# Optimization experiments

Measured on AMD Instinct MI355X. Metric: run time of the kernel, lower is better.

The kernel has to match this reference:

```python
import jax, jax.numpy as jnp
import numpy as np

# Module / grid constants (match init_kwargs and chosen input scale)
B, H, W = 2, 512, 512
SIZE, NIN, NOUT = 3, 64, 64
STRIDE, INV_STRIDE = 1, 1
N_NZ = 131072   # active input cells
N_MASK = 131072 # active output (mask) cells


def setup_inputs() -> dict:
    key = jax.random.key(0)
    ks = jax.random.split(key, 10)
    values = jax.random.normal(ks[0], (N_NZ, NIN), dtype=jnp.float32)
    # init matches torch: uniform in [-stdv, stdv]
    stdv = 1.0 / np.sqrt(float(SIZE * SIZE * NIN))
    kernel = (jax.random.uniform(ks[1], (SIZE, SIZE, NIN, NOUT), dtype=jnp.float32) - 0.5) * 2.0 * stdv
    bias = (jax.random.uniform(ks[2], (NOUT,), dtype=jnp.float32) - 0.5) * 2.0 * stdv
    ib = jax.random.randint(ks[3], (N_NZ,), 0, B)
    iy = jax.random.randint(ks[4], (N_NZ,), 0, H)
    ix = jax.random.randint(ks[5], (N_NZ,), 0, W)
    indices = jnp.stack([ib, iy, ix], axis=1).astype(jnp.int64)  # [N,3] like input.indices().T
    mb = jax.random.randint(ks[6], (N_MASK,), 0, B)
    my = jax.random.randint(ks[7], (N_MASK,), 0, H * INV_STRIDE // STRIDE)
    mx = jax.random.randint(ks[8], (N_MASK,), 0, W * INV_STRIDE // STRIDE)
    mask_indices = jnp.stack([mb, my, mx], axis=1).astype(jnp.int64)
    mask_values = jnp.ones((N_MASK, 1), dtype=jnp.float32)
    return {"values": values, "kernel": kernel, "bias": bias,
            "mask_values": mask_values, "indices": indices, "mask_indices": mask_indices}


def reference(values, kernel, bias, mask_values, indices, mask_indices):
    # Sparse octree conv: per kernel tap, gather-matmul-scatter with index
    # shift/scale and clamping to the output grid (clamped taps pile up on
    # the border exactly as torch.maximum/minimum do in the original).
    Ho = H // STRIDE * INV_STRIDE
    Wo = W // STRIDE * INV_STRIDE
    half = SIZE // 2
    b = indices[:, 0]
    dense = jnp.zeros((B, Ho, Wo, NOUT), dtype=values.dtype)
    for ky in range(SIZE):
        for kx in range(SIZE):
            v = values @ kernel[ky, kx]  # [N, nout]
            sy = jnp.clip((indices[:, 1] * INV_STRIDE + (ky - half)) // STRIDE, 0, Ho - 1)
            sx = jnp.clip((indices[:, 2] * INV_STRIDE + (kx - half)) // STRIDE, 0, Wo - 1)
            dense = dense.at[b, sy, sx].add(v)  # scatter-add == coalesce-sum
    # densified mask (duplicates sum, matching COO coalesce semantics)
    mask = jnp.zeros((B, Ho, Wo, 1), dtype=values.dtype)
    mask = mask.at[mask_indices[:, 0], mask_indices[:, 1], mask_indices[:, 2]].add(mask_values)
    # result = (result + mask * bias) * mask  (with_bias=True, mask nonempty)
    out = (dense + mask * bias) * mask
    return out
```

## Files before the change

### kernel.cpp

```cpp
#include <hip/hip_runtime.h>

#define BATCH 2
#define HH 512
#define WW 512
#define NIN 64
#define NOUT 64
#define N_NZ 131072
#define N_MASK 131072
#define NPIX (BATCH * HH * WW)
#define PPW 64
#define MAX_ALIVE N_MASK

#define WS_MASK_OFF   256
#define WS_SLOT_OFF   (WS_MASK_OFF + (size_t)NPIX * 4)
#define WS_CMP_OFF    (WS_SLOT_OFF + (size_t)NPIX * 4)
#define WS_NEED       (WS_CMP_OFF + (size_t)MAX_ALIVE * NOUT * 4)

__global__ void mask_scatter_kernel(const float* __restrict__ mv,
                                    const int* __restrict__ midx,
                                    float* __restrict__ mask) {
    int n = blockIdx.x * blockDim.x + threadIdx.x;
    if (n < N_MASK) {
        int b = midx[n * 3 + 0];
        int y = midx[n * 3 + 1];
        int x = midx[n * 3 + 2];
        atomicAdd(&mask[(b * HH + y) * WW + x], mv[n]);
    }
}

__global__ __launch_bounds__(256) void build_slot2_kernel(
        const float* __restrict__ mask,
        int* __restrict__ slot,
        int* __restrict__ counter) {
    const int tid = threadIdx.x;
    const int gid = blockIdx.x * 256 + tid;
    const float4 m = reinterpret_cast<const float4*>(mask)[gid];
    const int c0 = (m.x != 0.f) + (m.y != 0.f) + (m.z != 0.f) + (m.w != 0.f);

    const int lane = tid & 63;
    const int wv = tid >> 6;
    int pre = c0;
#pragma unroll
    for (int d = 1; d < 64; d <<= 1) {
        int t = __shfl_up(pre, d);
        if (lane >= d) pre += t;
    }

    __shared__ int wsum[4];
    __shared__ int wbase[4];
    __shared__ int blockbase;
    if (lane == 63) wsum[wv] = pre;
    __syncthreads();
    if (tid == 0) {
        int s = 0;
#pragma unroll
        for (int w = 0; w < 4; ++w) { wbase[w] = s; s += wsum[w]; }
        blockbase = atomicAdd(counter, s);
    }
    __syncthreads();

    int s0 = blockbase + wbase[wv] + (pre - c0);
    int4 sv;
    sv.x = (m.x != 0.f) ? s0++ : -1;
    sv.y = (m.y != 0.f) ? s0++ : -1;
    sv.z = (m.z != 0.f) ? s0++ : -1;
    sv.w = (m.w != 0.f) ? s0++ : -1;
    reinterpret_cast<int4*>(slot)[gid] = sv;
}

__global__ __launch_bounds__(64, 2) void conv_scatter2_kernel(
        const float* __restrict__ values,
        const float* __restrict__ kern,
        const int* __restrict__ idx,
        const int* __restrict__ slot,
        float* __restrict__ compact) {
    const int bid  = blockIdx.x;
    const int tap  = bid % 9;
    const int tile = bid / 9;
    const int lane = threadIdx.x;
    const int ky = tap / 3;
    const int kx = tap % 3;

    float kreg[NIN];
    const float* kp = kern + (size_t)tap * NIN * NOUT + lane;
#pragma unroll
    for (int i = 0; i < NIN; ++i) kreg[i] = kp[(size_t)i * NOUT];

    const int p0 = tile * PPW;
    const int p  = p0 + lane;
    const int b = idx[p * 3 + 0];
    const int y = idx[p * 3 + 1];
    const int x = idx[p * 3 + 2];
    const int sy = min(max(y + ky - 1, 0), HH - 1);
    const int sx = min(max(x + kx - 1, 0), WW - 1);
    const int pix = (b * HH + sy) * WW + sx;
    const int s = slot[pix];

    unsigned long long alive = __ballot(s >= 0);
    while (alive) {
        const int j = __ffsll((long long)alive) - 1;
        alive &= alive - 1;
        const int sj = __shfl(s, j);
        const float* vp = values + (size_t)(p0 + j) * NIN;
        float acc = 0.0f;
#pragma unroll
        for (int i = 0; i < NIN; ++i) acc = fmaf(vp[i], kreg[i], acc);
        atomicAdd(&compact[(size_t)sj * NOUT + lane], acc);
    }
}

__global__ void finalize2_kernel(float* __restrict__ out,
                                 const float* __restrict__ mask,
                                 const int* __restrict__ slot,
                                 const float* __restrict__ compact,
                                 const float* __restrict__ bias) {
    const int t = blockIdx.x * blockDim.x + threadIdx.x;
    const int p = t >> 4;
    const int c4 = (t & 15) * 4;
    if (p >= NPIX) return;
    float4* o = reinterpret_cast<float4*>(out + (size_t)p * NOUT + c4);
    const int s = slot[p];
    if (s < 0) {
        *o = make_float4(0.f, 0.f, 0.f, 0.f);
        return;
    }
    const float m = mask[p];
    const float4 bb = *reinterpret_cast<const float4*>(bias + c4);
    float4 v = *reinterpret_cast<const float4*>(compact + (size_t)s * NOUT + c4);
    v.x = (v.x + m * bb.x) * m;
    v.y = (v.y + m * bb.y) * m;
    v.z = (v.z + m * bb.z) * m;
    v.w = (v.w + m * bb.w) * m;
    *o = v;
}

__global__ __launch_bounds__(64, 2) void conv_scatter_kernel(
        const float* __restrict__ values,
        const float* __restrict__ kern,
        const int* __restrict__ idx,
        const float* __restrict__ mask,
        float* __restrict__ dense) {
    const int bid  = blockIdx.x;
    const int tap  = bid % 9;
    const int tile = bid / 9;
    const int lane = threadIdx.x;
    const int ky = tap / 3;
    const int kx = tap % 3;
    float kreg[NIN];
    const float* kp = kern + (size_t)tap * NIN * NOUT + lane;
#pragma unroll
    for (int i = 0; i < NIN; ++i) kreg[i] = kp[(size_t)i * NOUT];
    const int p0 = tile * PPW;
    for (int pp = 0; pp < PPW; ++pp) {
        const int p = p0 + pp;
        const int b = idx[p * 3 + 0];
        const int y = idx[p * 3 + 1];
        const int x = idx[p * 3 + 2];
        const int sy = min(max(y + ky - 1, 0), HH - 1);
        const int sx = min(max(x + kx - 1, 0), WW - 1);
        const size_t pix = ((size_t)b * HH + sy) * WW + sx;
        if (mask[pix] != 0.0f) {
            const float* vp = values + (size_t)p * NIN;
            float acc = 0.0f;
#pragma unroll
            for (int i = 0; i < NIN; ++i) acc = fmaf(vp[i], kreg[i], acc);
            atomicAdd(&dense[pix * NOUT + lane], acc);
        }
    }
}

__global__ void finalize_kernel(float* __restrict__ out,
                                const float* __restrict__ mask,
                                const float* __restrict__ bias) {
    const int t = blockIdx.x * blockDim.x + threadIdx.x;
    const int p = t >> 4;
    const int c4 = (t & 15) * 4;
    if (p >= NPIX) return;
    const float m = mask[p];
    if (m == 0.0f) return;
    float4* o = reinterpret_cast<float4*>(out + (size_t)p * NOUT + c4);
    const float4 bb = *reinterpret_cast<const float4*>(bias + c4);
    float4 v = *o;
    v.x = (v.x + m * bb.x) * m;
    v.y = (v.y + m * bb.y) * m;
    v.z = (v.z + m * bb.z) * m;
    v.w = (v.w + m * bb.w) * m;
    *o = v;
}

extern "C" void kernel_launch(void* const* d_in, const int* in_sizes, int n_in,
                              void* d_out, int out_size, void* d_ws, size_t ws_size,
                              hipStream_t stream) {
    const float* values      = (const float*)d_in[0];
    const float* kern        = (const float*)d_in[1];
    const float* bias        = (const float*)d_in[2];
    const float* mask_values = (const float*)d_in[3];
    const int*   indices     = (const int*)d_in[4];
    const int*   mask_idx    = (const int*)d_in[5];
    float* out = (float*)d_out;

    if (ws_size >= WS_NEED) {
        char* ws = (char*)d_ws;
        int*   counter = (int*)ws;
        float* mask    = (float*)(ws + WS_MASK_OFF);
        int*   slot    = (int*)(ws + WS_SLOT_OFF);
        float* compact = (float*)(ws + WS_CMP_OFF);

        hipMemsetAsync(ws, 0, WS_NEED, stream);

        mask_scatter_kernel<<<(N_MASK + 255) / 256, 256, 0, stream>>>(
            mask_values, mask_idx, mask);
        build_slot2_kernel<<<NPIX / 4 / 256, 256, 0, stream>>>(
            mask, slot, counter);

        const int nblocks = 9 * (N_NZ / PPW);
        conv_scatter2_kernel<<<nblocks, 64, 0, stream>>>(
            values, kern, indices, slot, compact);

        const int total = NPIX * (NOUT / 4);
        finalize2_kernel<<<(total + 255) / 256, 256, 0, stream>>>(
            out, mask, slot, compact, bias);
    } else {
        float* mask = (float*)d_ws;
        hipMemsetAsync(out, 0, (size_t)out_size * sizeof(float), stream);
        hipMemsetAsync(mask, 0, (size_t)NPIX * sizeof(float), stream);
        mask_scatter_kernel<<<(N_MASK + 255) / 256, 256, 0, stream>>>(
            mask_values, mask_idx, mask);
        const int nblocks = 9 * (N_NZ / PPW);
        conv_scatter_kernel<<<nblocks, 64, 0, stream>>>(
            values, kern, indices, mask, out);
        const int total = NPIX * (NOUT / 4);
        finalize_kernel<<<(total + 255) / 256, 256, 0, stream>>>(out, mask, bias);
    }
}
```

Measured before the change: 267.2 us.

## Compute per-tap gather GEMMs with bf16 MFMA, converting weights once per launch

Replaces the per-tap scalar FMA kernel with a single kernel in which each wave loads 16 input rows once, converts them to bf16, and loops over all 9 taps. For each tap it runs 16x16x32 bf16 MFMAs against a pre-transposed bf16 kernel, then atomically scatters the results to compact output slots. Taps where no row in the wave hits an active output are skipped. This removes the redundant per-tap reloads of values and the scalar FMA work, but lowers input precision to bf16 and adds a small weight-conversion kernel.

```diff
diff --git a/kernel.cpp b/kernel.cpp
--- a/kernel.cpp
+++ b/kernel.cpp
@@ -8,13 +8,23 @@
 #define N_NZ 131072
 #define N_MASK 131072
 #define NPIX (BATCH * HH * WW)
-#define PPW 64
 #define MAX_ALIVE N_MASK
 
 #define WS_MASK_OFF   256
 #define WS_SLOT_OFF   (WS_MASK_OFF + (size_t)NPIX * 4)
 #define WS_CMP_OFF    (WS_SLOT_OFF + (size_t)NPIX * 4)
-#define WS_NEED       (WS_CMP_OFF + (size_t)MAX_ALIVE * NOUT * 4)
+#define WS_KT_OFF     (WS_CMP_OFF + (size_t)MAX_ALIVE * NOUT * 4)
+#define WS_NEED2      (WS_KT_OFF + (size_t)9 * NIN * NOUT * 2)
+#define WS_NEED_R5    WS_KT_OFF
+
+typedef short s8v  __attribute__((ext_vector_type(8)));
+typedef float f4v  __attribute__((ext_vector_type(4)));
+
+__device__ __forceinline__ short f2bf(float f) {
+    unsigned u = __builtin_bit_cast(unsigned, f);
+    unsigned r = u + 0x7FFFu + ((u >> 16) & 1u);
+    return (short)(r >> 16);
+}
 
 __global__ void mask_scatter_kernel(const float* __restrict__ mv,
                                     const int* __restrict__ midx,
@@ -68,44 +78,89 @@
     reinterpret_cast<int4*>(slot)[gid] = sv;
 }
 
-__global__ __launch_bounds__(64, 2) void conv_scatter2_kernel(
+__global__ void convert_kt_kernel(const float* __restrict__ kern,
+                                  short* __restrict__ kt) {
+    int t = blockIdx.x * 256 + threadIdx.x;
+    if (t < 9 * NIN * NOUT) {
+        int tap = t >> 12;
+        int rem = t & 4095;
+        int c = rem >> 6;
+        int i = rem & 63;
+        kt[tap * 4096 + c * 64 + i] = f2bf(kern[tap * 4096 + i * 64 + c]);
+    }
+}
+
+__global__ __launch_bounds__(256) void conv_mfma_kernel(
         const float* __restrict__ values,
-        const float* __restrict__ kern,
+        const short* __restrict__ kt,
         const int* __restrict__ idx,
         const int* __restrict__ slot,
         float* __restrict__ compact) {
-    const int bid  = blockIdx.x;
-    const int tap  = bid % 9;
-    const int tile = bid / 9;
-    const int lane = threadIdx.x;
-    const int ky = tap / 3;
-    const int kx = tap % 3;
-
-    float kreg[NIN];
-    const float* kp = kern + (size_t)tap * NIN * NOUT + lane;
-#pragma unroll
-    for (int i = 0; i < NIN; ++i) kreg[i] = kp[(size_t)i * NOUT];
-
-    const int p0 = tile * PPW;
-    const int p  = p0 + lane;
-    const int b = idx[p * 3 + 0];
-    const int y = idx[p * 3 + 1];
-    const int x = idx[p * 3 + 2];
-    const int sy = min(max(y + ky - 1, 0), HH - 1);
-    const int sx = min(max(x + kx - 1, 0), WW - 1);
-    const int pix = (b * HH + sy) * WW + sx;
-    const int s = slot[pix];
-
-    unsigned long long alive = __ballot(s >= 0);
-    while (alive) {
-        const int j = __ffsll((long long)alive) - 1;
-        alive &= alive - 1;
-        const int sj = __shfl(s, j);
-        const float* vp = values + (size_t)(p0 + j) * NIN;
-        float acc = 0.0f;
-#pragma unroll
-        for (int i = 0; i < NIN; ++i) acc = fmaf(vp[i], kreg[i], acc);
-        atomicAdd(&compact[(size_t)sj * NOUT + lane], acc);
+    const int wid  = threadIdx.x >> 6;
+    const int lane = threadIdx.x & 63;
+    const int q    = lane >> 4;
+    const int col  = lane & 15;
+    const int p0   = blockIdx.x * 64 + wid * 16;
+
+    const float* vrow = values + (size_t)(p0 + col) * NIN + q * 8;
+    s8v a0, a1;
+#pragma unroll
+    for (int j = 0; j < 8; ++j) {
+        a0[j] = f2bf(vrow[j]);
+        a1[j] = f2bf(vrow[32 + j]);
+    }
+
+    const int pme = p0 + col;
+    const int b = idx[pme * 3 + 0];
+    const int y = idx[pme * 3 + 1];
+    const int x = idx[pme * 3 + 2];
+
+    for (int tap = 0; tap < 9; ++tap) {
+        const int ky = tap / 3;
+        const int kx = tap % 3;
+        const int sy = min(max(y + ky - 1, 0), HH - 1);
+        const int sx = min(max(x + kx - 1, 0), WW - 1);
+        const int s = slot[(b * HH + sy) * WW + sx];
+
+        if (__ballot(s >= 0) == 0ULL) continue;
+
+        const short* ktt = kt + tap * 4096;
+        const short* kb = ktt + col * 64 + q * 8;
+
+        f4v c0 = {0.f, 0.f, 0.f, 0.f};
+        f4v c1 = {0.f, 0.f, 0.f, 0.f};
+        f4v c2 = {0.f, 0.f, 0.f, 0.f};
+        f4v c3 = {0.f, 0.f, 0.f, 0.f};
+
+        s8v b0a = *(const s8v*)(kb + 0 * 16 * 64);
+        s8v b0b = *(const s8v*)(kb + 0 * 16 * 64 + 32);
+        c0 = __builtin_amdgcn_mfma_f32_16x16x32_bf16(a0, b0a, c0, 0, 0, 0);
+        c0 = __builtin_amdgcn_mfma_f32_16x16x32_bf16(a1, b0b, c0, 0, 0, 0);
+        s8v b1a = *(const s8v*)(kb + 1 * 16 * 64);
+        s8v b1b = *(const s8v*)(kb + 1 * 16 * 64 + 32);
+        c1 = __builtin_amdgcn_mfma_f32_16x16x32_bf16(a0, b1a, c1, 0, 0, 0);
+        c1 = __builtin_amdgcn_mfma_f32_16x16x32_bf16(a1, b1b, c1, 0, 0, 0);
+        s8v b2a = *(const s8v*)(kb + 2 * 16 * 64);
+        s8v b2b = *(const s8v*)(kb + 2 * 16 * 64 + 32);
+        c2 = __builtin_amdgcn_mfma_f32_16x16x32_bf16(a0, b2a, c2, 0, 0, 0);
+        c2 = __builtin_amdgcn_mfma_f32_16x16x32_bf16(a1, b2b, c2, 0, 0, 0);
+        s8v b3a = *(const s8v*)(kb + 3 * 16 * 64);
+        s8v b3b = *(const s8v*)(kb + 3 * 16 * 64 + 32);
+        c3 = __builtin_amdgcn_mfma_f32_16x16x32_bf16(a0, b3a, c3, 0, 0, 0);
+        c3 = __builtin_amdgcn_mfma_f32_16x16x32_bf16(a1, b3b, c3, 0, 0, 0);
+
+#pragma unroll
+        for (int r = 0; r < 4; ++r) {
+            const int mr = q * 4 + r;
+            const int sr = __shfl(s, mr);
+            if (sr >= 0) {
+                float* dst = compact + (size_t)sr * NOUT + col;
+                atomicAdd(dst + 0,  c0[r]);
+                atomicAdd(dst + 16, c1[r]);
+                atomicAdd(dst + 32, c2[r]);
+                atomicAdd(dst + 48, c3[r]);
+            }
+        }
     }
 }
 
@@ -134,12 +189,12 @@
     *o = v;
 }
 
-__global__ __launch_bounds__(64, 2) void conv_scatter_kernel(
+__global__ __launch_bounds__(64, 2) void conv_scatter3_kernel(
         const float* __restrict__ values,
         const float* __restrict__ kern,
         const int* __restrict__ idx,
-        const float* __restrict__ mask,
-        float* __restrict__ dense) {
+        const int* __restrict__ slot,
+        float* __restrict__ compact) {
     const int bid  = blockIdx.x;
     const int tap  = bid % 9;
     const int tile = bid / 9;
@@ -150,42 +205,26 @@
     const float* kp = kern + (size_t)tap * NIN * NOUT + lane;
 #pragma unroll
     for (int i = 0; i < NIN; ++i) kreg[i] = kp[(size_t)i * NOUT];
-    const int p0 = tile * PPW;
-    for (int pp = 0; pp < PPW; ++pp) {
-        const int p = p0 + pp;
-        const int b = idx[p * 3 + 0];
-        const int y = idx[p * 3 + 1];
-        const int x = idx[p * 3 + 2];
-        const int sy = min(max(y + ky - 1, 0), HH - 1);
-        const int sx = min(max(x + kx - 1, 0), WW - 1);
-        const size_t pix = ((size_t)b * HH + sy) * WW + sx;
-        if (mask[pix] != 0.0f) {
-            const float* vp = values + (size_t)p * NIN;
-            float acc = 0.0f;
-#pragma unroll
-            for (int i = 0; i < NIN; ++i) acc = fmaf(vp[i], kreg[i], acc);
-            atomicAdd(&dense[pix * NOUT + lane], acc);
-        }
-    }
-}
-
-__global__ void finalize_kernel(float* __restrict__ out,
-                                const float* __restrict__ mask,
-                                const float* __restrict__ bias) {
-    const int t = blockIdx.x * blockDim.x + threadIdx.x;
-    const int p = t >> 4;
-    const int c4 = (t & 15) * 4;
-    if (p >= NPIX) return;
-    const float m = mask[p];
-    if (m == 0.0f) return;
-    float4* o = reinterpret_cast<float4*>(out + (size_t)p * NOUT + c4);
-    const float4 bb = *reinterpret_cast<const float4*>(bias + c4);
-    float4 v = *o;
-    v.x = (v.x + m * bb.x) * m;
-    v.y = (v.y + m * bb.y) * m;
-    v.z = (v.z + m * bb.z) * m;
-    v.w = (v.w + m * bb.w) * m;
-    *o = v;
+    const int p0 = tile * 64;
+    const int p  = p0 + lane;
+    const int b = idx[p * 3 + 0];
+    const int y = idx[p * 3 + 1];
+    const int x = idx[p * 3 + 2];
+    const int sy = min(max(y + ky - 1, 0), HH - 1);
+    const int sx = min(max(x + kx - 1, 0), WW - 1);
+    const int pix = (b * HH + sy) * WW + sx;
+    const int s = slot[pix];
+    unsigned long long alive = __ballot(s >= 0);
+    while (alive) {
+        const int j = __ffsll((long long)alive) - 1;
+        alive &= alive - 1;
+        const int sj = __shfl(s, j);
+        const float* vp = values + (size_t)(p0 + j) * NIN;
+        float acc = 0.0f;
+#pragma unroll
+        for (int i = 0; i < NIN; ++i) acc = fmaf(vp[i], kreg[i], acc);
+        atomicAdd(&compact[(size_t)sj * NOUT + lane], acc);
+    }
 }
 
 extern "C" void kernel_launch(void* const* d_in, const int* in_sizes, int n_in,
@@ -199,37 +238,34 @@
     const int*   mask_idx    = (const int*)d_in[5];
     float* out = (float*)d_out;
 
-    if (ws_size >= WS_NEED) {
-        char* ws = (char*)d_ws;
-        int*   counter = (int*)ws;
-        float* mask    = (float*)(ws + WS_MASK_OFF);
-        int*   slot    = (int*)(ws + WS_SLOT_OFF);
-        float* compact = (float*)(ws + WS_CMP_OFF);
-
-        hipMemsetAsync(ws, 0, WS_NEED, stream);
-
-        mask_scatter_kernel<<<(N_MASK + 255) / 256, 256, 0, stream>>>(
-            mask_values, mask_idx, mask);
-        build_slot2_kernel<<<NPIX / 4 / 256, 256, 0, stream>>>(
-            mask, slot, counter);
-
-        const int nblocks = 9 * (N_NZ / PPW);
-        conv_scatter2_kernel<<<nblocks, 64, 0, stream>>>(
+    char* ws = (char*)d_ws;
+    int*   counter = (int*)ws;
+    float* mask    = (float*)(ws + WS_MASK_OFF);
+    int*   slot    = (int*)(ws + WS_SLOT_OFF);
+    float* compact = (float*)(ws + WS_CMP_OFF);
+    short* kt      = (short*)(ws + WS_KT_OFF);
+
+    const bool mfma_path = (ws_size >= WS_NEED2);
+    const size_t zero_span = mfma_path ? WS_NEED2 : WS_NEED_R5;
+
+    hipMemsetAsync(ws, 0, zero_span, stream);
+
+    mask_scatter_kernel<<<(N_MASK + 255) / 256, 256, 0, stream>>>(
+        mask_values, mask_idx, mask);
+    build_slot2_kernel<<<NPIX / 4 / 256, 256, 0, stream>>>(
+        mask, slot, counter);
+
+    if (mfma_path) {
+        convert_kt_kernel<<<(9 * NIN * NOUT + 255) / 256, 256, 0, stream>>>(
+            kern, kt);
+        conv_mfma_kernel<<<N_NZ / 64, 256, 0, stream>>>(
+            values, kt, indices, slot, compact);
+    } else {
+        conv_scatter3_kernel<<<9 * (N_NZ / 64), 64, 0, stream>>>(
             values, kern, indices, slot, compact);
-
-        const int total = NPIX * (NOUT / 4);
-        finalize2_kernel<<<(total + 255) / 256, 256, 0, stream>>>(
-            out, mask, slot, compact, bias);
-    } else {
-        float* mask = (float*)d_ws;
-        hipMemsetAsync(out, 0, (size_t)out_size * sizeof(float), stream);
-        hipMemsetAsync(mask, 0, (size_t)NPIX * sizeof(float), stream);
-        mask_scatter_kernel<<<(N_MASK + 255) / 256, 256, 0, stream>>>(
-            mask_values, mask_idx, mask);
-        const int nblocks = 9 * (N_NZ / PPW);
-        conv_scatter_kernel<<<nblocks, 64, 0, stream>>>(
-            values, kern, indices, mask, out);
-        const int total = NPIX * (NOUT / 4);
-        finalize_kernel<<<(total + 255) / 256, 256, 0, stream>>>(out, mask, bias);
-    }
-}
+    }
+
+    const int total = NPIX * (NOUT / 4);
+    finalize2_kernel<<<(total + 255) / 256, 256, 0, stream>>>(
+        out, mask, slot, compact, bias);
+}
```

Result: no change. 266.8 us (-0.2%).
